# Optimization experiments

Measured on AMD Instinct MI355X. Metric: run time of the kernel, lower is better.

## Reference

```python
import jax, jax.numpy as jnp
import numpy as np
from jax import lax

B, N, NUM_CLASSES = 16, 48384, 1
CONF_THRESH = 0.25
IOU_THRESH = 0.45
MAX_PER_IMG = 100
K = 512           # NMS candidate pool (top-K by score)
IMG_SIZE = 1536.0
CLS_OFFSET = 4096.0  # class-aware NMS offset trick


def setup_inputs() -> dict:
    key = jax.random.key(0)
    k1, k2, k3 = jax.random.split(key, 3)
    # cx, cy in [0, IMG), w, h in [0, 0.2*IMG)
    coords = jax.random.uniform(k1, (B, N, 4)) * jnp.array(
        [IMG_SIZE, IMG_SIZE, 0.2 * IMG_SIZE, 0.2 * IMG_SIZE], dtype=jnp.float32)
    confs = jax.random.uniform(k2, (B, N, 1 + NUM_CLASSES))  # obj + class scores in [0,1)
    pred_boxes = jnp.concatenate([coords, confs], axis=-1)   # [B, N, 6]
    features = jax.random.normal(k3, (B, 256, 48, 48), dtype=jnp.float32)
    return {"pred_boxes": pred_boxes, "features": features}


def _iou_matrix(boxes):
    # boxes: [K, 4] xyxy -> [K, K] pairwise IoU
    area = jnp.clip(boxes[:, 2] - boxes[:, 0], 0.0) * jnp.clip(boxes[:, 3] - boxes[:, 1], 0.0)
    lt = jnp.maximum(boxes[:, None, :2], boxes[None, :, :2])
    rb = jnp.minimum(boxes[:, None, 2:], boxes[None, :, 2:])
    wh = jnp.clip(rb - lt, 0.0)
    inter = wh[..., 0] * wh[..., 1]
    return inter / (area[:, None] + area[None, :] - inter + 1e-9)


def _find_thresh(scores, t0):
    # Retry loop of the wrapper: lower conf_thresh until >=1 box passes the conf mask.
    s = lax.stop_gradient(scores)
    def cond(t):
        return jnp.sum(s >= t) == 0
    def body(t):
        return jnp.maximum(t - 0.1, t / 10.0)
    return lax.while_loop(cond, body, t0)


def _postprocess_one(pred, thresh):
    # pred: [N, 5+num_classes]
    cx, cy, w, h = pred[:, 0], pred[:, 1], pred[:, 2], pred[:, 3]
    boxes = jnp.stack([cx - w / 2, cy - h / 2, cx + w / 2, cy + h / 2], axis=-1)  # xyxy
    obj = pred[:, 4]
    cls = pred[:, 5:]
    class_conf = jnp.max(cls, axis=-1)
    class_pred = jnp.argmax(cls, axis=-1)
    score = obj * class_conf
    valid = score >= thresh
    cand_score, idx = lax.top_k(jnp.where(valid, score, 0.0), K)
    cboxes = boxes[idx]
    ccls = class_pred[idx]
    cobj = obj[idx]
    cconf = class_conf[idx]
    cvalid = valid[idx]
    # class-aware NMS: offset boxes per class so cross-class pairs never overlap
    off = ccls.astype(boxes.dtype) * CLS_OFFSET
    iou = _iou_matrix(cboxes + off[:, None])  # [K, K]
    ar = jnp.arange(K)
    def body(i, keep):
        sup = keep[i] & (iou[i] > IOU_THRESH) & (ar > i)
        return keep & ~sup
    keep = lax.fori_loop(0, K, body, cvalid)  # greedy NMS (candidates sorted desc)
    final = jnp.where(keep, cand_score, 0.0)
    out_score, oidx = lax.top_k(final, MAX_PER_IMG)
    det = jnp.concatenate(
        [cboxes[oidx], cobj[oidx][:, None], cconf[oidx][:, None],
         ccls[oidx][:, None].astype(boxes.dtype)], axis=-1)  # [max_det, 7]
    kmask = keep[oidx]
    det = jnp.where(kmask[:, None], det, 0.0)
    return det, kmask


def reference(pred_boxes, features):
    obj = pred_boxes[..., 4]
    cconf = jnp.max(pred_boxes[..., 5:], axis=-1)
    scores = obj * cconf  # [B, N]
    t0 = jnp.full((pred_boxes.shape[0],), CONF_THRESH, pred_boxes.dtype)
    thresh = jax.vmap(_find_thresh)(scores, t0)
    det, mask = jax.vmap(_postprocess_one)(pred_boxes, thresh)
    return det, mask, features
```

## Files before the change

kernel.cpp:

```cpp
#include <hip/hip_runtime.h>
#include <stdint.h>

typedef unsigned int u32;
typedef unsigned long long u64;

#define BATCH 16
#define NBOX  48384
#define KC    512
#define MAXDET 100
#define CONF_T 0.25f
#define HCUT   0.75f
#define IOU_T  0.45f
#define DET_FLOATS (BATCH*MAXDET*7)
#define MASK_OFF   DET_FLOATS
#define FEAT_OFF   (DET_FLOATS + BATCH*MAXDET)
#define FEAT_N     (BATCH*256*48*48)
#define FEAT4_N    (FEAT_N/4)

#define CAPH  4096
#define HBUF  160
#define NBINS 64
#define NBLK1 64
#define BOXPB 756
#define NF4   (BOXPB*6/4)
#define K1COPYB 512

__device__ __forceinline__ u64 xorred_u64(u64 v, int m){
    u32 lo = __shfl_xor((u32)(v & 0xFFFFFFFFull), m, 64);
    u32 hi = __shfl_xor((u32)(v >> 32), m, 64);
    return ((u64)hi << 32) | lo;
}
__device__ __forceinline__ u64 shflxor_u64(u64 v, int j){
    u32 lo = __shfl_xor((u32)(v & 0xFFFFFFFFull), j, 64);
    u32 hi = __shfl_xor((u32)(v >> 32), j, 64);
    return ((u64)hi << 32) | lo;
}
__device__ __forceinline__ int score_bin(float sc){
    int bin = (int)((sc - 0.75f) * 256.0f);
    return bin > 63 ? 63 : bin;
}

__global__ __launch_bounds__(512) void k1_score(const float* __restrict__ pred,
        u64* __restrict__ hkey, u32* __restrict__ blkcnt, u32* __restrict__ ghist,
        float* __restrict__ blkmax, const float4* __restrict__ feat4,
        float* __restrict__ out, int copyB)
{
    __shared__ float s_t[BOXPB*6];
    __shared__ u64 s_hb[HBUF];
    __shared__ u32 s_hist[NBINS];
    __shared__ u32 s_hc;
    __shared__ float s_wm[8];

    const int tid = threadIdx.x;

    if ((int)blockIdx.x < copyB){
        const int nthr = copyB * 512;
        float4* dst = reinterpret_cast<float4*>(out + FEAT_OFF);
        for (int i = (int)blockIdx.x*512 + tid; i < FEAT4_N; i += nthr)
            dst[i] = feat4[i];
        return;
    }

    const int sid = (int)blockIdx.x - copyB;
    const int b = sid >> 6, blk = sid & 63;
    if (tid == 0) s_hc = 0u;
    if (tid < NBINS) s_hist[tid] = 0u;

    const float4* src = (const float4*)(pred + ((size_t)b*NBOX + blk*BOXPB)*6);
    #pragma unroll
    for (int i = tid; i < NF4; i += 512) ((float4*)s_t)[i] = src[i];
    __syncthreads();

    float m = 0.f;
    for (int i = tid; i < BOXPB; i += 512){
        const float2 oc = *(const float2*)&s_t[i*6+4];
        const float sc = oc.x * oc.y;
        m = fmaxf(m, sc);
        if (sc >= HCUT){
            const u32 slot = atomicAdd(&s_hc, 1u);
            const u32 idx = (u32)(blk*BOXPB + i);
            if (slot < (u32)HBUF)
                s_hb[slot] = ((u64)__float_as_uint(sc) << 32) | (u64)(0xFFFFFFFFu - idx);
            atomicAdd(&s_hist[score_bin(sc)], 1u);
        }
    }
    #pragma unroll
    for (int off = 32; off >= 1; off >>= 1) m = fmaxf(m, __shfl_xor(m, off, 64));
    if ((tid & 63) == 0) s_wm[tid >> 6] = m;
    __syncthreads();
    if (tid == 0){
        float mm = s_wm[0];
        #pragma unroll
        for (int w = 1; w < 8; w++) mm = fmaxf(mm, s_wm[w]);
        blkmax[sid] = mm;
        blkcnt[sid] = s_hc;
    }
    if (tid < NBINS) ghist[(size_t)sid*NBINS + tid] = s_hist[tid];
    const u32 hn = (s_hc < (u32)HBUF ? s_hc : (u32)HBUF);
    for (u32 i = tid; i < hn; i += 512)
        hkey[(size_t)sid*HBUF + i] = s_hb[i];
}

__global__ void copy_kernel(const float4* __restrict__ src, float4* __restrict__ dst){
    int stride = gridDim.x * blockDim.x;
    for (int i = blockIdx.x*blockDim.x + threadIdx.x; i < FEAT4_N; i += stride)
        dst[i] = src[i];
}

__global__ __launch_bounds__(1024) void k2a_sel(
        const float* __restrict__ pred, const u64* __restrict__ hkey,
        const u32* __restrict__ blkcnt, u32* ghist ,
        const float* __restrict__ blkmax)
{
    __shared__ u64 s_list[CAPH];
    __shared__ u64 s_key[KC];
    __shared__ u32 s_scr[1024];
    __shared__ u64 s_tie[256];
    __shared__ u32 s_eqidx[256];
    __shared__ u32 s_pfx[64], s_cnt[64];
    __shared__ float s_thresh;
    __shared__ u32 s_Mh, s_maxc, s_pivbin, s_need, s_fastok;
    __shared__ u32 s_prefix, s_k, s_cntgt, s_cnteq;
    __shared__ int s_vM;

    const int tid = threadIdx.x;
    const int b = blockIdx.x;
    const float* predb = pred + (size_t)b*NBOX*6;

    {
        if (tid < 64){
            float vv = blkmax[b*NBLK1 + tid];
            #pragma unroll
            for (int off = 32; off >= 1; off >>= 1) vv = fmaxf(vv, __shfl_xor(vv, off, 64));
            if (tid == 0){
                float t = CONF_T; int g = 0;
                while (vv < t && g < 256){ t = fmaxf(t - 0.1f, t * 0.1f); g++; }
                s_thresh = t;
                s_cntgt = 0u; s_cnteq = 0u; s_fastok = 0u;
            }
        } else if (tid < 128){
            const int l = tid - 64;
            u32 c = blkcnt[b*NBLK1 + l];
            s_cnt[l] = c;
            u32 p = c;
            #pragma unroll
            for (int off = 1; off < 64; off <<= 1){
                u32 o = __shfl_up(p, off, 64);
                if (l >= off) p += o;
            }
            s_pfx[l] = p - c;
            u32 mc = c;
            #pragma unroll
            for (int off = 32; off >= 1; off >>= 1) mc = (u32)max(mc, __shfl_xor(mc, off, 64));
            if (l == 63) s_Mh = p;
            if (l == 0)  s_maxc = mc;
        }
    }
    __syncthreads();
    const u32 Mh = s_Mh;
    const bool fastm = (Mh >= (u32)KC) && (Mh <= (u32)CAPH) && (s_maxc <= (u32)HBUF);

    if (fastm){
        const int wv = tid >> 6, ln = tid & 63;
        #pragma unroll
        for (int q = 0; q < 4; q++){
            const int s = wv + q*16;
            const u32 n = s_cnt[s], base = s_pfx[s];
            const u64* src = hkey + (size_t)(b*NBLK1 + s)*HBUF;
            for (u32 i = ln; i < n; i += 64) s_list[base + i] = src[i];
        }
        const int j = tid & 63, g = tid >> 6;
        const u32* gh = ghist + (size_t)b*NBLK1*NBINS;
        s_scr[g*64 + j] = gh[(g     )*64 + j] + gh[(g + 16)*64 + j]
                        + gh[(g + 32)*64 + j] + gh[(g + 48)*64 + j];
    }
    __syncthreads();
    if (fastm && tid < 64){
        u32 h = 0;
        #pragma unroll
        for (int g = 0; g < 16; g++) h += s_scr[g*64 + tid];
        u32 c = h;
        #pragma unroll
        for (int off = 1; off < 64; off <<= 1){
            u32 o = __shfl_down(c, off, 64);
            c += (tid + off < 64) ? o : 0u;
        }
        const u32 above = c - h;
        if (above < (u32)KC && above + h >= (u32)KC){
            s_pivbin = (u32)tid;
            s_need = (u32)KC - above;
            s_fastok = (h <= 256u) ? 1u : 0u;
        }
    }
    __syncthreads();
    const bool fsel = fastm && (s_fastok != 0u);

    if (fsel){
        const u32 pb = s_pivbin;
        for (u32 i = tid; i < Mh; i += 1024){
            const u64 key = s_list[i];
            const float sc = __uint_as_float((u32)(key >> 32));
            const u32 j2 = (u32)score_bin(sc);
            if (j2 > pb){
                u32 sl = atomicAdd(&s_cntgt, 1u);
                if (sl < (u32)KC) s_key[sl] = key;
            } else if (j2 == pb){
                u32 e = atomicAdd(&s_cnteq, 1u);
                if (e < 256u) s_tie[e] = key;
            }
        }
        __syncthreads();
        {
            const u32 g0v = (s_cntgt < (u32)KC) ? s_cntgt : (u32)KC;
            u32 ecv = (s_cnteq < 256u) ? s_cnteq : 256u;
            u32 needv = (s_need < ecv) ? s_need : ecv;
            if (tid < (int)ecv){
                const u64 me = s_tie[tid];
                u32 r = 0;
                for (u32 u2 = 0; u2 < ecv; ++u2) r += (s_tie[u2] > me) ? 1u : 0u;
                if (r < needv && g0v + r < (u32)KC) s_key[g0v + r] = me;
            }
            for (int i = (int)(g0v + needv) + tid; i < KC; i += 1024) s_key[i] = 0ull;
        }
        __syncthreads();
    } else {
        const float thresh = s_thresh;
        const u32 base8 = __float_as_uint(thresh) >> 24;
        u32 (*s_hist4)[256] = reinterpret_cast<u32(*)[256]>(s_scr);
        {
            u64 c0=0, c1=0, c2=0, c3=0;
            for (int i = tid; i < NBOX; i += 1024){
                const float* pp = predb + (size_t)i*6;
                float sc = pp[4] * pp[5];
                if (sc >= thresh){
                    u32 d = (__float_as_uint(sc) >> 24) - base8; if (d > 15u) d = 15u;
                    u64 inc = 1ull << (16*(d & 3u)); u32 q = d >> 2;
                    c0 += (q==0u)?inc:0ull; c1 += (q==1u)?inc:0ull;
                    c2 += (q==2u)?inc:0ull; c3 += (q==3u)?inc:0ull;
                }
            }
            #pragma unroll
            for (int off = 32; off >= 1; off >>= 1){
                c0 += xorred_u64(c0,off); c1 += xorred_u64(c1,off);
                c2 += xorred_u64(c2,off); c3 += xorred_u64(c3,off);
            }
            u64* warr = s_key;
            if ((tid & 63) == 0){
                int w = tid >> 6;
                warr[w*4+0]=c0; warr[w*4+1]=c1; warr[w*4+2]=c2; warr[w*4+3]=c3;
            }
            __syncthreads();
            if (tid < 16){
                u32 tot = 0;
                #pragma unroll
                for (int w = 0; w < 16; w++){
                    u64 vv = warr[w*4 + (tid >> 2)];
                    tot += (u32)((vv >> (16*(tid & 3))) & 0xFFFFull);
                }
                s_hist4[0][tid] = tot;
            }
            __syncthreads();
            if (tid == 0){
                u32 h[16]; u32 tot = 0;
                #pragma unroll
                for (int d = 0; d < 16; d++){ h[d] = s_hist4[0][d]; tot += h[d]; }
                s_vM = (int)tot;
                s_k = KC; s_prefix = 0u;
                if (tot > (u32)KC){
                    u32 k = KC, c = 0; int d = 15;
                    for (; d >= 0; --d){ if (c + h[d] >= k) break; c += h[d]; }
                    if (d < 0) d = 0;
                    s_prefix = (base8 + (u32)d) << 24; s_k = k - c;
                }
            }
            __syncthreads();
        }
        const int vM = s_vM;
        if (vM > KC){
            for (int shift = 16; shift >= 0; shift -= 8){
                ((u32*)s_hist4)[tid] = 0u;
                __syncthreads();
                const u32 prefix = s_prefix;
                const u32 pmask = 0xFFFFFFFFu << (shift + 8);
                const int cpy = tid >> 8;
                for (int i = tid; i < NBOX; i += 1024){
                    const float* pp = predb + (size_t)i*6;
                    float sc = pp[4] * pp[5];
                    if (sc >= thresh){
                        u32 bb = __float_as_uint(sc);
                        if ((bb & pmask) == (prefix & pmask))
                            atomicAdd(&s_hist4[cpy][(bb >> shift) & 0xFFu], 1u);
                    }
                }
                __syncthreads();
                if (tid < 256)
                    s_hist4[0][tid] = s_hist4[0][tid] + s_hist4[1][tid]
                                    + s_hist4[2][tid] + s_hist4[3][tid];
                __syncthreads();
                if (tid < 64){
                    const int l = tid;
                    u32 h0 = s_hist4[0][4*l+0], h1 = s_hist4[0][4*l+1];
                    u32 h2 = s_hist4[0][4*l+2], h3 = s_hist4[0][4*l+3];
                    u32 mysum = h0+h1+h2+h3;
                    u32 c = mysum;
                    #pragma unroll
                    for (int off = 1; off < 64; off <<= 1){
                        u32 o = __shfl_down(c, off, 64);
                        c += (l + off < 64) ? o : 0u;
                    }
                    u32 a3 = c - mysum;
                    u32 a2 = a3 + h3, a1 = a2 + h2, a0 = a1 + h1;
                    u32 k = s_k;
                    int sel = -1; u32 cab = 0;
                    if (a0 < k && a0 + h0 >= k){ sel = 0; cab = a0; }
                    if (a1 < k && a1 + h1 >= k){ sel = 1; cab = a1; }
                    if (a2 < k && a2 + h2 >= k){ sel = 2; cab = a2; }
                    if (a3 < k && a3 + h3 >= k){ sel = 3; cab = a3; }
                    if (sel >= 0){
                        s_prefix = prefix | ((u32)(4*l + sel) << shift);
                        s_k = k - cab;
                    }
                }
                __syncthreads();
            }
        }
        const u32 pivot = (vM > KC) ? s_prefix : 0u;
        const bool pivot0 = (vM <= KC);
        const int kneed = pivot0 ? 0 : (int)s_k;
        for (int i = tid; i < NBOX; i += 1024){
            const float* pp = predb + (size_t)i*6;
            float sc = pp[4] * pp[5];
            if (sc < thresh) continue;
            u32 bb = __float_as_uint(sc);
            if (bb > pivot){
                u32 sl = atomicAdd(&s_cntgt, 1u);
                if (sl < (u32)KC) s_key[sl] = ((u64)bb << 32) | (u64)(0xFFFFFFFFu - (u32)i);
            } else if (!pivot0 && bb == pivot){
                u32 e = atomicAdd(&s_cnteq, 1u);
                if (e < 256u) s_eqidx[e] = (u32)i;
            }
        }
        __syncthreads();
        if (tid == 0){
            int g = (int)s_cntgt; if (g > KC) g = KC;
            int ec = (int)s_cnteq; if (ec > 256) ec = 256;
            int need = kneed < ec ? kneed : ec;
            for (int t = 0; t < need; t++){
                int mi = t;
                for (int u = t+1; u < ec; u++) if (s_eqidx[u] < s_eqidx[mi]) mi = u;
                u32 tmp = s_eqidx[mi]; s_eqidx[mi] = s_eqidx[t]; s_eqidx[t] = tmp;
                if (g < KC) s_key[g++] = ((u64)pivot << 32) | (u64)(0xFFFFFFFFu - tmp);
            }
            while (g < KC) s_key[g++] = 0ull;
        }
        __syncthreads();
    }

    u64 v = (tid < KC) ? s_key[tid] : 0ull;
    {
        #define CAS_W(kk, j) \
            if (tid < KC){ \
                u64 p = shflxor_u64(v, (j)); \
                bool keepMax = (((tid & (kk)) == 0) == ((tid & (j)) == 0)); \
                u64 mx = (v > p) ? v : p, mn = (v > p) ? p : v; \
                v = keepMax ? mx : mn; \
            }
        #define CAS_L(kk, j) \
            __syncthreads(); \
            if (tid < KC) s_key[tid] = v; \
            __syncthreads(); \
            if (tid < KC){ \
                u64 p = s_key[tid ^ (j)]; \
                bool keepMax = (((tid & (kk)) == 0) == ((tid & (j)) == 0)); \
                u64 mx = (v > p) ? v : p, mn = (v > p) ? p : v; \
                v = keepMax ? mx : mn; \
            }
        CAS_W(2,1)
        CAS_W(4,2)  CAS_W(4,1)
        CAS_W(8,4)  CAS_W(8,2)  CAS_W(8,1)
        CAS_W(16,8) CAS_W(16,4) CAS_W(16,2) CAS_W(16,1)
        CAS_W(32,16) CAS_W(32,8) CAS_W(32,4) CAS_W(32,2) CAS_W(32,1)
        CAS_W(64,32) CAS_W(64,16) CAS_W(64,8) CAS_W(64,4) CAS_W(64,2) CAS_W(64,1)
        CAS_L(128,64)
        CAS_W(128,32) CAS_W(128,16) CAS_W(128,8) CAS_W(128,4) CAS_W(128,2) CAS_W(128,1)
        CAS_L(256,128) CAS_L(256,64)
        CAS_W(256,32) CAS_W(256,16) CAS_W(256,8) CAS_W(256,4) CAS_W(256,2) CAS_W(256,1)
        CAS_L(512,256) CAS_L(512,128) CAS_L(512,64)
        CAS_W(512,32) CAS_W(512,16) CAS_W(512,8) CAS_W(512,4) CAS_W(512,2) CAS_W(512,1)
        #undef CAS_W
        #undef CAS_L
    }

    if (tid < KC){
        u32 bb = (u32)(v >> 32);
        u32 idx = 0xFFFFFFFFu - (u32)(v & 0xFFFFFFFFull);
        int srcrow = (bb != 0u) ? (int)idx : 0;
        const float* p = predb + (size_t)srcrow*6;
        float cx = p[0], cy = p[1], w = p[2], h = p[3], ob = p[4], cf = p[5];
        float x1 = cx - w * 0.5f, y1 = cy - h * 0.5f;
        float x2 = cx + w * 0.5f, y2 = cy + h * 0.5f;
        float4* cw = reinterpret_cast<float4*>(ghist) + ((size_t)b*KC + tid)*2;
        cw[0] = make_float4(x1, y1, x2, y2);
        cw[1] = make_float4(fmaxf(x2 - x1, 0.f) * fmaxf(y2 - y1, 0.f),
                            ob, cf, __uint_as_float(bb));
    }
}

__global__ __launch_bounds__(576) void k2b_iou(const float4* __restrict__ cand,
                                               u64* __restrict__ masks)
{
    __shared__ float4 s_box[KC];
    __shared__ float s_area[KC];
    const int tid = threadIdx.x;
    const int b = (int)blockIdx.x >> 2, q = (int)blockIdx.x & 3;
    const float4* cb = cand + (size_t)b*KC*2;

    for (int i = tid; i < KC; i += 576){
        s_box[i] = cb[2*i];
        s_area[i] = cb[2*i+1].x;
    }
    __syncthreads();

    const int wv = tid >> 6, lane = tid & 63;
    const int p = q*9 + wv;
    int d = 0; while ((d+1)*(d+2)/2 <= p) d++;
    const int c = p - d*(d+1)/2;
    const int j = d*64 + lane;
    const float4 bj = s_box[j];
    const float aj = s_area[j];
    u64 acc = 0ull;
    for (int t = 0; t < 64; t++){
        const float4 bi = s_box[c*64 + t];
        const float ai = s_area[c*64 + t];
        float lx = fmaxf(bi.x, bj.x), ly = fmaxf(bi.y, bj.y);
        float rx = fminf(bi.z, bj.z), ry = fminf(bi.w, bj.w);
        float iw = fmaxf(rx - lx, 0.f), ih = fmaxf(ry - ly, 0.f);
        float inter = iw * ih;
        float denom = ai + aj - inter + 1e-9f;
        bool sup = (inter > IOU_T * denom) && (c < d || t < lane);
        acc |= sup ? (1ull << t) : 0ull;
    }
    masks[(size_t)b*4096 + (size_t)c*512 + j] = acc;
}

__global__ __launch_bounds__(512) void k2c_nms(const float4* __restrict__ cand,
        const u64* __restrict__ masks, float* __restrict__ out)
{
    __shared__ u64 s_masks[8];
    __shared__ u32 s_wpcnt[8], s_wpfx[8];
    __shared__ int s_outidx[MAXDET];
    __shared__ int s_outcnt;

    const int tid = threadIdx.x;
    const int b = blockIdx.x;
    const int wave = tid >> 6, lane = tid & 63;
    const float4* cb = cand + (size_t)b*KC*2;
    const u64* mb = masks + (size_t)b*4096;

    const float4 meta = cb[2*tid + 1];
    bool alive = (__float_as_uint(meta.w) != 0u);
    const u64 diag = mb[(size_t)wave*512 + tid];
    u64 pre[7];
    #pragma unroll
    for (int e = 0; e < 7; e++) pre[e] = (e < wave) ? mb[(size_t)e*512 + tid] : 0ull;

    for (int c = 0; c < 8; c++){
        if (wave == c){
            #pragma unroll
            for (int e = 0; e < 7; e++)
                if (e < c) alive = alive && ((pre[e] & s_masks[e]) == 0ull);
            for (int t = 0; t < 64; t++){
                u64 mnow = __ballot(alive);
                bool at = (mnow >> t) & 1ull;
                alive = alive && !(at && ((diag >> t) & 1ull));
            }
            u64 fin = __ballot(alive);
            if (lane == 0) s_masks[c] = fin;
        }
        __syncthreads();
    }

    if (tid < 8) s_wpcnt[tid] = (u32)__popcll(s_masks[tid]);
    __syncthreads();
    if (tid == 0){
        u32 run = 0;
        #pragma unroll
        for (int w = 0; w < 8; w++){ s_wpfx[w] = run; run += s_wpcnt[w]; }
        s_outcnt = (int)(run < MAXDET ? run : MAXDET);
    }
    __syncthreads();
    {
        const u64 wd = s_masks[wave];
        if ((wd >> lane) & 1ull){
            u32 rank = s_wpfx[wave] + (u32)__popcll(wd & ((1ull << lane) - 1ull));
            if (rank < MAXDET) s_outidx[rank] = tid;
        }
    }
    __syncthreads();
    if (tid < MAXDET){
        const int obase = (b * MAXDET + tid) * 7;
        if (tid < s_outcnt){
            int c = s_outidx[tid];
            float4 bx = cb[2*c];
            float4 mt = cb[2*c + 1];
            out[obase+0] = bx.x; out[obase+1] = bx.y;
            out[obase+2] = bx.z; out[obase+3] = bx.w;
            out[obase+4] = mt.y; out[obase+5] = mt.z;
            out[obase+6] = 0.f;
            out[MASK_OFF + b*MAXDET + tid] = 1.f;
        } else {
            #pragma unroll
            for (int q = 0; q < 7; q++) out[obase+q] = 0.f;
            out[MASK_OFF + b*MAXDET + tid] = 0.f;
        }
    }
}

extern "C" void kernel_launch(void* const* d_in, const int* in_sizes, int n_in,
                              void* d_out, int out_size, void* d_ws, size_t ws_size,
                              hipStream_t stream) {
    (void)in_sizes; (void)n_in; (void)out_size;
    const float* pred = (const float*)d_in[0];
    const float* feat = (const float*)d_in[1];
    float* out = (float*)d_out;

    const size_t hkeyBytes = (size_t)BATCH * NBLK1 * HBUF * 8;
    const size_t cntBytes  = (size_t)BATCH * NBLK1 * 4;
    const size_t histBytes = (size_t)BATCH * NBLK1 * NBINS * 4;
    const size_t maxBytes  = (size_t)BATCH * NBLK1 * 4;
    const size_t needBytes = hkeyBytes + cntBytes + histBytes + maxBytes;

    char* base; bool fused;
    if (ws_size >= needBytes){ base = (char*)d_ws; fused = true; }
    else { base = (char*)(out + FEAT_OFF); fused = false; }

    u64* hkeyp  = (u64*)base;
    u32* blkcnt = (u32*)(base + hkeyBytes);
    u32* ghist  = (u32*)(base + hkeyBytes + cntBytes);
    float* blkmax = (float*)(base + hkeyBytes + cntBytes + histBytes);
    float4* cand = (float4*)ghist;
    u64* masks   = hkeyp;

    if (fused){
        k1_score<<<dim3(K1COPYB + BATCH*NBLK1), dim3(512), 0, stream>>>(
            pred, hkeyp, blkcnt, ghist, blkmax, (const float4*)feat, out, K1COPYB);
        k2a_sel<<<dim3(BATCH), dim3(1024), 0, stream>>>(pred, hkeyp, blkcnt, ghist, blkmax);
        k2b_iou<<<dim3(BATCH*4), dim3(576), 0, stream>>>(cand, masks);
        k2c_nms<<<dim3(BATCH), dim3(512), 0, stream>>>(cand, masks, out);
    } else {
        k1_score<<<dim3(BATCH*NBLK1), dim3(512), 0, stream>>>(
            pred, hkeyp, blkcnt, ghist, blkmax, (const float4*)feat, out, 0);
        k2a_sel<<<dim3(BATCH), dim3(1024), 0, stream>>>(pred, hkeyp, blkcnt, ghist, blkmax);
        k2b_iou<<<dim3(BATCH*4), dim3(576), 0, stream>>>(cand, masks);
        k2c_nms<<<dim3(BATCH), dim3(512), 0, stream>>>(cand, masks, out);
        copy_kernel<<<dim3(1024), dim3(256), 0, stream>>>(
            (const float4*)feat, (float4*)(out + FEAT_OFF));
    }
}
```

Before: 149.6 us.

## Spread feature copy across all kernels and speed up NMS and selection paths

The feature-map passthrough copy is split into four slices, each handled by extra blocks appended to one of the four kernel launches, so the copy overlaps the latency-bound single-batch stages instead of only running beside k1. The intra-wave greedy NMS now keeps an alive bitmask and applies diagonal suppression masks broadcast by shuffle, replacing a ballot per step; the diagonal masks are written to a separate buffer with upper-triangle orientation. Selection compaction uses wave ballots and one atomic per wave instead of per-thread atomics, k1 reads pred directly instead of staging it through shared memory, and the candidate gather uses float2 loads. These changes add extra blocks to small kernels and rely on the vmasks region fitting inside the workspace.

```diff
diff --git a/kernel.cpp b/kernel.cpp
--- a/kernel.cpp
+++ b/kernel.cpp
@@ -22,8 +22,15 @@
 #define NBINS 64
 #define NBLK1 64
 #define BOXPB 756
-#define NF4   (BOXPB*6/4)
-#define K1COPYB 512
+
+#define F64   (FEAT4_N/64)
+#define CSL1  (13*F64)
+#define CSL2  (45*F64)
+#define CSL3  (54*F64)
+#define K1CPB  256
+#define K2ACPB 240
+#define K2BCPB 192
+#define K2CCPB 240
 
 __device__ __forceinline__ u64 xorred_u64(u64 v, int m){
     u32 lo = __shfl_xor((u32)(v & 0xFFFFFFFFull), m, 64);
@@ -33,6 +40,11 @@
 __device__ __forceinline__ u64 shflxor_u64(u64 v, int j){
     u32 lo = __shfl_xor((u32)(v & 0xFFFFFFFFull), j, 64);
     u32 hi = __shfl_xor((u32)(v >> 32), j, 64);
+    return ((u64)hi << 32) | lo;
+}
+__device__ __forceinline__ u64 shflidx_u64(u64 v, int src){
+    u32 lo = (u32)__shfl((int)(u32)(v & 0xFFFFFFFFull), src, 64);
+    u32 hi = (u32)__shfl((int)(u32)(v >> 32), src, 64);
     return ((u64)hi << 32) | lo;
 }
 __device__ __forceinline__ int score_bin(float sc){
@@ -45,7 +57,6 @@
         float* __restrict__ blkmax, const float4* __restrict__ feat4,
         float* __restrict__ out, int copyB)
 {
-    __shared__ float s_t[BOXPB*6];
     __shared__ u64 s_hb[HBUF];
     __shared__ u32 s_hist[NBINS];
     __shared__ u32 s_hc;
@@ -56,7 +67,7 @@
     if ((int)blockIdx.x < copyB){
         const int nthr = copyB * 512;
         float4* dst = reinterpret_cast<float4*>(out + FEAT_OFF);
-        for (int i = (int)blockIdx.x*512 + tid; i < FEAT4_N; i += nthr)
+        for (int i = (int)blockIdx.x*512 + tid; i < CSL1; i += nthr)
             dst[i] = feat4[i];
         return;
     }
@@ -65,15 +76,12 @@
     const int b = sid >> 6, blk = sid & 63;
     if (tid == 0) s_hc = 0u;
     if (tid < NBINS) s_hist[tid] = 0u;
-
-    const float4* src = (const float4*)(pred + ((size_t)b*NBOX + blk*BOXPB)*6);
-    #pragma unroll
-    for (int i = tid; i < NF4; i += 512) ((float4*)s_t)[i] = src[i];
-    __syncthreads();
-
+    __syncthreads();
+
+    const float* pb = pred + ((size_t)b*NBOX + (size_t)blk*BOXPB)*6;
     float m = 0.f;
     for (int i = tid; i < BOXPB; i += 512){
-        const float2 oc = *(const float2*)&s_t[i*6+4];
+        const float2 oc = *(const float2*)(pb + (size_t)i*6 + 4);
         const float sc = oc.x * oc.y;
         m = fmaxf(m, sc);
         if (sc >= HCUT){
@@ -110,7 +118,8 @@
 __global__ __launch_bounds__(1024) void k2a_sel(
         const float* __restrict__ pred, const u64* __restrict__ hkey,
         const u32* __restrict__ blkcnt, u32* ghist ,
-        const float* __restrict__ blkmax)
+        const float* __restrict__ blkmax,
+        const float4* __restrict__ feat4, float* __restrict__ out, int copyB)
 {
     __shared__ u64 s_list[CAPH];
     __shared__ u64 s_key[KC];
@@ -124,6 +133,15 @@
     __shared__ int s_vM;
 
     const int tid = threadIdx.x;
+
+    if ((int)blockIdx.x >= BATCH){
+        const int nthr = copyB * 1024;
+        float4* dst = reinterpret_cast<float4*>(out + FEAT_OFF);
+        for (int i = CSL1 + ((int)blockIdx.x - BATCH)*1024 + tid; i < CSL2; i += nthr)
+            dst[i] = feat4[i];
+        return;
+    }
+
     const int b = blockIdx.x;
     const float* predb = pred + (size_t)b*NBOX*6;
 
@@ -197,15 +215,33 @@
 
     if (fsel){
         const u32 pb = s_pivbin;
-        for (u32 i = tid; i < Mh; i += 1024){
-            const u64 key = s_list[i];
-            const float sc = __uint_as_float((u32)(key >> 32));
-            const u32 j2 = (u32)score_bin(sc);
-            if (j2 > pb){
-                u32 sl = atomicAdd(&s_cntgt, 1u);
+        const u32 lane = (u32)(tid & 63);
+        const u64 below = (1ull << lane) - 1ull;
+        for (u32 i0 = 0; i0 < Mh; i0 += 1024){
+            const u32 i = i0 + (u32)tid;
+            const bool inr = (i < Mh);
+            const u64 key = inr ? s_list[i] : 0ull;
+            u32 j2 = 0u;
+            if (inr){
+                const float sc = __uint_as_float((u32)(key >> 32));
+                j2 = (u32)score_bin(sc);
+            }
+            const bool isgt = inr && (j2 > pb);
+            const bool iseq = inr && (j2 == pb);
+            const u64 mg = __ballot(isgt);
+            const u64 me = __ballot(iseq);
+            u32 bg = 0u, be = 0u;
+            if (lane == 0u){
+                bg = atomicAdd(&s_cntgt, (u32)__popcll(mg));
+                be = atomicAdd(&s_cnteq, (u32)__popcll(me));
+            }
+            bg = (u32)__shfl((int)bg, 0, 64);
+            be = (u32)__shfl((int)be, 0, 64);
+            if (isgt){
+                const u32 sl = bg + (u32)__popcll(mg & below);
                 if (sl < (u32)KC) s_key[sl] = key;
-            } else if (j2 == pb){
-                u32 e = atomicAdd(&s_cnteq, 1u);
+            } else if (iseq){
+                const u32 e = be + (u32)__popcll(me & below);
                 if (e < 256u) s_tie[e] = key;
             }
         }
@@ -215,10 +251,10 @@
             u32 ecv = (s_cnteq < 256u) ? s_cnteq : 256u;
             u32 needv = (s_need < ecv) ? s_need : ecv;
             if (tid < (int)ecv){
-                const u64 me = s_tie[tid];
+                const u64 me2 = s_tie[tid];
                 u32 r = 0;
-                for (u32 u2 = 0; u2 < ecv; ++u2) r += (s_tie[u2] > me) ? 1u : 0u;
-                if (r < needv && g0v + r < (u32)KC) s_key[g0v + r] = me;
+                for (u32 u2 = 0; u2 < ecv; ++u2) r += (s_tie[u2] > me2) ? 1u : 0u;
+                if (r < needv && g0v + r < (u32)KC) s_key[g0v + r] = me2;
             }
             for (int i = (int)(g0v + needv) + tid; i < KC; i += 1024) s_key[i] = 0ull;
         }
@@ -396,7 +432,10 @@
         u32 idx = 0xFFFFFFFFu - (u32)(v & 0xFFFFFFFFull);
         int srcrow = (bb != 0u) ? (int)idx : 0;
         const float* p = predb + (size_t)srcrow*6;
-        float cx = p[0], cy = p[1], w = p[2], h = p[3], ob = p[4], cf = p[5];
+        const float2 p01 = *(const float2*)(p);
+        const float2 p23 = *(const float2*)(p + 2);
+        const float2 p45 = *(const float2*)(p + 4);
+        float cx = p01.x, cy = p01.y, w = p23.x, h = p23.y, ob = p45.x, cf = p45.y;
         float x1 = cx - w * 0.5f, y1 = cy - h * 0.5f;
         float x2 = cx + w * 0.5f, y2 = cy + h * 0.5f;
         float4* cw = reinterpret_cast<float4*>(ghist) + ((size_t)b*KC + tid)*2;
@@ -407,11 +446,21 @@
 }
 
 __global__ __launch_bounds__(576) void k2b_iou(const float4* __restrict__ cand,
-                                               u64* __restrict__ masks)
+        u64* __restrict__ masks, u64* __restrict__ vmasks,
+        const float4* __restrict__ feat4, float* __restrict__ out, int copyB)
 {
     __shared__ float4 s_box[KC];
     __shared__ float s_area[KC];
     const int tid = threadIdx.x;
+
+    if ((int)blockIdx.x >= BATCH*4){
+        const int nthr = copyB * 576;
+        float4* dst = reinterpret_cast<float4*>(out + FEAT_OFF);
+        for (int i = CSL2 + ((int)blockIdx.x - BATCH*4)*576 + tid; i < CSL3; i += nthr)
+            dst[i] = feat4[i];
+        return;
+    }
+
     const int b = (int)blockIdx.x >> 2, q = (int)blockIdx.x & 3;
     const float4* cb = cand + (size_t)b*KC*2;
 
@@ -428,6 +477,7 @@
     const int j = d*64 + lane;
     const float4 bj = s_box[j];
     const float aj = s_area[j];
+    const bool isdiag = (c == d);
     u64 acc = 0ull;
     for (int t = 0; t < 64; t++){
         const float4 bi = s_box[c*64 + t];
@@ -437,14 +487,18 @@
         float iw = fmaxf(rx - lx, 0.f), ih = fmaxf(ry - ly, 0.f);
         float inter = iw * ih;
         float denom = ai + aj - inter + 1e-9f;
-        bool sup = (inter > IOU_T * denom) && (c < d || t < lane);
-        acc |= sup ? (1ull << t) : 0ull;
-    }
-    masks[(size_t)b*4096 + (size_t)c*512 + j] = acc;
+        const bool iouc = (inter > IOU_T * denom);
+        bool setb = isdiag ? (iouc && t > lane) : iouc;
+        acc |= setb ? (1ull << t) : 0ull;
+    }
+    if (isdiag) vmasks[(size_t)b*KC + c*64 + lane] = acc;
+    else        masks[(size_t)b*4096 + (size_t)c*512 + j] = acc;
 }
 
 __global__ __launch_bounds__(512) void k2c_nms(const float4* __restrict__ cand,
-        const u64* __restrict__ masks, float* __restrict__ out)
+        const u64* __restrict__ masks, const u64* __restrict__ vmasks,
+        float* __restrict__ out,
+        const float4* __restrict__ feat4, int copyB)
 {
     __shared__ u64 s_masks[8];
     __shared__ u32 s_wpcnt[8], s_wpfx[8];
@@ -452,30 +506,40 @@
     __shared__ int s_outcnt;
 
     const int tid = threadIdx.x;
+
+    if ((int)blockIdx.x >= BATCH){
+        const int nthr = copyB * 512;
+        float4* dst = reinterpret_cast<float4*>(out + FEAT_OFF);
+        for (int i = CSL3 + ((int)blockIdx.x - BATCH)*512 + tid; i < FEAT4_N; i += nthr)
+            dst[i] = feat4[i];
+        return;
+    }
+
     const int b = blockIdx.x;
     const int wave = tid >> 6, lane = tid & 63;
     const float4* cb = cand + (size_t)b*KC*2;
     const u64* mb = masks + (size_t)b*4096;
 
     const float4 meta = cb[2*tid + 1];
-    bool alive = (__float_as_uint(meta.w) != 0u);
-    const u64 diag = mb[(size_t)wave*512 + tid];
+    const bool alive0 = (__float_as_uint(meta.w) != 0u);
+    const u64 vm = vmasks[(size_t)b*KC + tid];
     u64 pre[7];
     #pragma unroll
     for (int e = 0; e < 7; e++) pre[e] = (e < wave) ? mb[(size_t)e*512 + tid] : 0ull;
 
     for (int c = 0; c < 8; c++){
         if (wave == c){
+            bool alive = alive0;
             #pragma unroll
             for (int e = 0; e < 7; e++)
                 if (e < c) alive = alive && ((pre[e] & s_masks[e]) == 0ull);
+            u64 A = __ballot(alive);
+            #pragma unroll
             for (int t = 0; t < 64; t++){
-                u64 mnow = __ballot(alive);
-                bool at = (mnow >> t) & 1ull;
-                alive = alive && !(at && ((diag >> t) & 1ull));
-            }
-            u64 fin = __ballot(alive);
-            if (lane == 0) s_masks[c] = fin;
+                const u64 m = shflidx_u64(vm, t);
+                if ((A >> t) & 1ull) A &= ~m;
+            }
+            if (lane == 0) s_masks[c] = A;
         }
         __syncthreads();
     }
@@ -540,19 +604,26 @@
     float* blkmax = (float*)(base + hkeyBytes + cntBytes + histBytes);
     float4* cand = (float4*)ghist;
     u64* masks   = hkeyp;
+    u64* vmasks  = hkeyp + (size_t)BATCH*4096;
 
     if (fused){
-        k1_score<<<dim3(K1COPYB + BATCH*NBLK1), dim3(512), 0, stream>>>(
-            pred, hkeyp, blkcnt, ghist, blkmax, (const float4*)feat, out, K1COPYB);
-        k2a_sel<<<dim3(BATCH), dim3(1024), 0, stream>>>(pred, hkeyp, blkcnt, ghist, blkmax);
-        k2b_iou<<<dim3(BATCH*4), dim3(576), 0, stream>>>(cand, masks);
-        k2c_nms<<<dim3(BATCH), dim3(512), 0, stream>>>(cand, masks, out);
+        k1_score<<<dim3(K1CPB + BATCH*NBLK1), dim3(512), 0, stream>>>(
+            pred, hkeyp, blkcnt, ghist, blkmax, (const float4*)feat, out, K1CPB);
+        k2a_sel<<<dim3(BATCH + K2ACPB), dim3(1024), 0, stream>>>(
+            pred, hkeyp, blkcnt, ghist, blkmax, (const float4*)feat, out, K2ACPB);
+        k2b_iou<<<dim3(BATCH*4 + K2BCPB), dim3(576), 0, stream>>>(
+            cand, masks, vmasks, (const float4*)feat, out, K2BCPB);
+        k2c_nms<<<dim3(BATCH + K2CCPB), dim3(512), 0, stream>>>(
+            cand, masks, vmasks, out, (const float4*)feat, K2CCPB);
     } else {
         k1_score<<<dim3(BATCH*NBLK1), dim3(512), 0, stream>>>(
             pred, hkeyp, blkcnt, ghist, blkmax, (const float4*)feat, out, 0);
-        k2a_sel<<<dim3(BATCH), dim3(1024), 0, stream>>>(pred, hkeyp, blkcnt, ghist, blkmax);
-        k2b_iou<<<dim3(BATCH*4), dim3(576), 0, stream>>>(cand, masks);
-        k2c_nms<<<dim3(BATCH), dim3(512), 0, stream>>>(cand, masks, out);
+        k2a_sel<<<dim3(BATCH), dim3(1024), 0, stream>>>(
+            pred, hkeyp, blkcnt, ghist, blkmax, (const float4*)feat, out, 0);
+        k2b_iou<<<dim3(BATCH*4), dim3(576), 0, stream>>>(
+            cand, masks, vmasks, (const float4*)feat, out, 0);
+        k2c_nms<<<dim3(BATCH), dim3(512), 0, stream>>>(
+            cand, masks, vmasks, out, (const float4*)feat, 0);
         copy_kernel<<<dim3(1024), dim3(256), 0, stream>>>(
             (const float4*)feat, (float4*)(out + FEAT_OFF));
     }
```

Result: faster. 135.4 us (-9.5%).
